# Kernel tuning notes

Measured on AMD Instinct MI355X. Metric: run time of the kernel, lower is better.

## Reference

```python
import jax, jax.numpy as jnp
import numpy as np


def setup_inputs() -> dict:
    key = jax.random.key(0)
    k1, k2, k3, k4, k5 = jax.random.split(key, 5)
    B, S, D, H, E = 4, 4096, 1024, 1024, 8  # H = per-expert hidden (fuel_dim)
    std = 0.02
    return {
        "hidden_states": jax.random.normal(k1, (B, S, D), dtype=jnp.float32),
        "gate_w": jax.random.normal(k2, (D, E), dtype=jnp.float32) * std,
        "gw": jax.random.normal(k3, (E, D, H), dtype=jnp.float32) * std,
        "pw": jax.random.normal(k4, (E, D, H), dtype=jnp.float32) * std,
        "ow": jax.random.normal(k5, (E, H, D), dtype=jnp.float32) * std,
        "top_k": 2,
    }


def reference(hidden_states, gate_w, gw, pw, ow, top_k):
    B, S, D = hidden_states.shape
    E = gate_w.shape[1]
    x = hidden_states.reshape(-1, D)  # [T, D]
    T = x.shape[0]

    # Router
    router_logits = x @ gate_w  # [T, E]
    routing_probs = jax.nn.softmax(router_logits.astype(jnp.float32), axis=-1)
    top_w, top_i = jax.lax.top_k(routing_probs, top_k)  # [T, k]
    top_w = top_w / jnp.sum(top_w, axis=-1, keepdims=True)
    top_w = top_w.astype(x.dtype)

    # Dense combine weights: zero for unselected experts -> same math as
    # the torch gather/expert/scatter loop.
    combine = jnp.zeros((T, E), dtype=x.dtype).at[
        jnp.arange(T)[:, None], top_i
    ].set(top_w)  # [T, E]

    # SwiGLU experts, batched over the expert dim.
    g = jnp.einsum('td,edh->eth', x, gw)          # [E, T, H]
    p = jnp.einsum('td,edh->eth', x, pw)          # [E, T, H]
    h = g * jax.nn.silu(p)                        # [E, T, H]
    y = jnp.einsum('eth,ehd->etd', h, ow)         # [E, T, D]
    final = jnp.einsum('etd,te->td', y, combine)  # [T, D]
    final = final.reshape(B, S, D)

    # Load-balancing loss (recomputes softmax/topk as the torch fn does)
    expert_mask = jax.nn.one_hot(top_i, E, dtype=jnp.float32)  # [T, k, E]
    tokens_per_expert = jnp.mean(expert_mask, axis=0)          # [k, E]
    router_prob_per_expert = jnp.mean(routing_probs, axis=0)   # [E]
    bl_loss = jnp.sum(tokens_per_expert * router_prob_per_expert[None, :]) * E

    return final, router_logits, bl_loss
```

## Files before the change

kernel.cpp:

```cpp
#include <hip/hip_runtime.h>
#include <hip/hip_bf16.h>
#include <cstdint>

#define T_TOK 16384
#define DDIM  1024

typedef __attribute__((ext_vector_type(8))) short bf16x8;
typedef __attribute__((ext_vector_type(4))) float f32x4;

__device__ __forceinline__ unsigned short f2bf(float f) {
  unsigned u = __builtin_bit_cast(unsigned, f);
  return (unsigned short)((u + 0x7fffu + ((u >> 16) & 1u)) >> 16);
}
__device__ __forceinline__ unsigned pk2(float a, float b) {
  return (unsigned)f2bf(a) | ((unsigned)f2bf(b) << 16);
}
__device__ __forceinline__ void gload16(const void* g, void* l) {
  typedef __attribute__((address_space(1))) const unsigned int gu32;
  typedef __attribute__((address_space(3))) unsigned int lu32;
  __builtin_amdgcn_global_load_lds((gu32*)g, (lu32*)l, 16, 0, 0);
}

#define SBAR()                        \
  __builtin_amdgcn_sched_barrier(0);  \
  __builtin_amdgcn_s_barrier();       \
  __builtin_amdgcn_sched_barrier(0)
#define WAIT_VM8()                                        \
  asm volatile("s_waitcnt vmcnt(8)" ::: "memory");        \
  __builtin_amdgcn_sched_barrier(0)
#define WAIT_VM0()                                        \
  asm volatile("s_waitcnt vmcnt(0)" ::: "memory");        \
  __builtin_amdgcn_sched_barrier(0)

__global__ __launch_bounds__(256) void convert_k(
    const float* __restrict__ gw, const float* __restrict__ pw,
    const float* __restrict__ ow, char* __restrict__ wg,
    char* __restrict__ wp, char* __restrict__ wo) {
  __shared__ float t[64][65];
  const int z = blockIdx.z;
  const int arr = z >> 3, e = z & 7;
  const float* src = (arr == 0 ? gw : arr == 1 ? pw : ow) + ((long)e << 20);
  char* dst = (arr == 0 ? wg : arr == 1 ? wp : wo) + ((long)e << 21);
  const int r0 = blockIdx.x * 64, c0 = blockIdx.y * 64;
  const int row = threadIdx.x >> 2, q = threadIdx.x & 3;
  const float4* sp = (const float4*)(src + (long)(r0 + row) * 1024 + c0 + q * 16);
  float4 v0 = sp[0], v1 = sp[1], v2 = sp[2], v3 = sp[3];
  float* tr = &t[row][q * 16];
  tr[0]=v0.x; tr[1]=v0.y; tr[2]=v0.z; tr[3]=v0.w;
  tr[4]=v1.x; tr[5]=v1.y; tr[6]=v1.z; tr[7]=v1.w;
  tr[8]=v2.x; tr[9]=v2.y; tr[10]=v2.z; tr[11]=v2.w;
  tr[12]=v3.x; tr[13]=v3.y; tr[14]=v3.z; tr[15]=v3.w;
  __syncthreads();
  const int cl = row, rq = q;
  uint4 o0, o1;
  o0.x = pk2(t[rq*16+ 0][cl], t[rq*16+ 1][cl]);
  o0.y = pk2(t[rq*16+ 2][cl], t[rq*16+ 3][cl]);
  o0.z = pk2(t[rq*16+ 4][cl], t[rq*16+ 5][cl]);
  o0.w = pk2(t[rq*16+ 6][cl], t[rq*16+ 7][cl]);
  o1.x = pk2(t[rq*16+ 8][cl], t[rq*16+ 9][cl]);
  o1.y = pk2(t[rq*16+10][cl], t[rq*16+11][cl]);
  o1.z = pk2(t[rq*16+12][cl], t[rq*16+13][cl]);
  o1.w = pk2(t[rq*16+14][cl], t[rq*16+15][cl]);
  char* dp = dst + (long)(c0 + cl) * 2048 + (long)(r0 + rq * 16) * 2;
  *(uint4*)dp = o0;
  *(uint4*)(dp + 16) = o1;
}

__global__ __launch_bounds__(256) void router_k(
    const float* __restrict__ x, const float* __restrict__ gatew,
    float* __restrict__ logitsOut, float4* __restrict__ route,
    float* __restrict__ accum, unsigned short* __restrict__ xbo) {
  __shared__ float accB[16];
  const int tid = threadIdx.x;
  if (tid < 16) accB[tid] = 0.f;
  __syncthreads();
  const int lane = tid & 63;
  const int gwave = blockIdx.x * 4 + (tid >> 6);

  for (int g = gwave; g < 4096; g += 1024) {
    const int t0 = g * 4;
    float s[4][8];
#pragma unroll
    for (int tt = 0; tt < 4; ++tt)
#pragma unroll
      for (int e = 0; e < 8; ++e) s[tt][e] = 0.f;

    for (int i = 0; i < 16; ++i) {
      int d = lane + i * 64;
      float4 w0 = *(const float4*)(gatew + d * 8);
      float4 w1 = *(const float4*)(gatew + d * 8 + 4);
#pragma unroll
      for (int tt = 0; tt < 4; ++tt) {
        float xv = x[(long)(t0 + tt) * DDIM + d];
        if (xbo) xbo[(long)(t0 + tt) * DDIM + d] = f2bf(xv);
        s[tt][0] += xv * w0.x; s[tt][1] += xv * w0.y;
        s[tt][2] += xv * w0.z; s[tt][3] += xv * w0.w;
        s[tt][4] += xv * w1.x; s[tt][5] += xv * w1.y;
        s[tt][6] += xv * w1.z; s[tt][7] += xv * w1.w;
      }
    }
#pragma unroll
    for (int m = 1; m < 64; m <<= 1)
#pragma unroll
      for (int tt = 0; tt < 4; ++tt)
#pragma unroll
        for (int e = 0; e < 8; ++e) s[tt][e] += __shfl_xor(s[tt][e], m);

    float psum[8];
#pragma unroll
    for (int e = 0; e < 8; ++e) psum[e] = 0.f;
    int i1a[4], i2a[4];
    float w1a[4], w2a[4];
#pragma unroll
    for (int tt = 0; tt < 4; ++tt) {
      float mx = s[tt][0];
#pragma unroll
      for (int e = 1; e < 8; ++e) mx = fmaxf(mx, s[tt][e]);
      float pe[8], Z = 0.f;
#pragma unroll
      for (int e = 0; e < 8; ++e) { pe[e] = __expf(s[tt][e] - mx); Z += pe[e]; }
      float inv = 1.f / Z;
#pragma unroll
      for (int e = 0; e < 8; ++e) { pe[e] *= inv; psum[e] += pe[e]; }
      int i1 = 0; float p1 = pe[0];
#pragma unroll
      for (int e = 1; e < 8; ++e) if (pe[e] > p1) { p1 = pe[e]; i1 = e; }
      int i2 = -1; float p2 = -1.f;
#pragma unroll
      for (int e = 0; e < 8; ++e)
        if (e != i1 && pe[e] > p2) { p2 = pe[e]; i2 = e; }
      float wsum = p1 + p2;
      i1a[tt] = i1; i2a[tt] = i2;
      w1a[tt] = p1 / wsum; w2a[tt] = p2 / wsum;
    }
    if (lane < 32) {
      int tt = lane >> 3, e = lane & 7;
      logitsOut[(t0 + tt) * 8 + e] = s[tt][e];
    }
    if (lane < 32 && (lane & 7) == 0) {
      int tt = lane >> 3;
      float4 rr;
      rr.x = w1a[tt]; rr.y = w2a[tt];
      rr.z = __int_as_float(i1a[tt]); rr.w = __int_as_float(i2a[tt]);
      route[t0 + tt] = rr;
    }
    if (lane < 8) {
      float c = 0.f;
#pragma unroll
      for (int tt = 0; tt < 4; ++tt)
        c += (float)(i1a[tt] == lane) + (float)(i2a[tt] == lane);
      atomicAdd(&accB[lane], psum[lane]);
      atomicAdd(&accB[8 + lane], c);
    }
  }
  __syncthreads();
  if (tid < 16) atomicAdd(&accum[tid], accB[tid]);
}

__global__ void offsets_k(const float* __restrict__ accum,
                          int* __restrict__ offs, int* __restrict__ cursor) {
  if (threadIdx.x == 0) {
    int c = 0;
#pragma unroll
    for (int e = 0; e < 8; ++e) {
      offs[e] = c; cursor[e] = c;
      c += (int)(accum[8 + e] + 0.5f);
    }
    offs[8] = c;
  }
}

__global__ __launch_bounds__(256) void scatter_k(
    const float4* __restrict__ route, int* __restrict__ cursor,
    int* __restrict__ list, float* __restrict__ wsl) {
  int t = blockIdx.x * 256 + threadIdx.x;
  float4 rr = route[t];
  int i1 = __float_as_int(rr.z), i2 = __float_as_int(rr.w);
  int s1 = atomicAdd(&cursor[i1], 1);
  list[s1] = t; wsl[s1] = rr.x;
  int s2 = atomicAdd(&cursor[i2], 1);
  list[s2] = t; wsl[s2] = rr.y;
}

template <int XB>
__global__ __launch_bounds__(512, 2) void pass1_k(
    const float* __restrict__ x, const unsigned short* __restrict__ xb,
    const char* __restrict__ wg, const char* __restrict__ wp,
    const int* __restrict__ list, const float* __restrict__ wsl,
    const int* __restrict__ offs, char* __restrict__ hw) {
  __shared__ __align__(16) char Al[2][32768];
  __shared__ __align__(16) char Bgl[2][16384];
  __shared__ __align__(16) char Bpl[2][16384];
  const int e = blockIdx.x & 7, tile = blockIdx.x >> 3;
  const int s0 = offs[e], s1 = offs[e + 1];
  const int start = s0 + tile * 256;
  if (start >= s1) return;
  const int valid = min(256, s1 - start);
  const int chunk = blockIdx.y;
  const int tid = threadIdx.x, lane = tid & 63, wid = tid >> 6;

  const int l8 = lane >> 3, seg = lane & 7;
  const unsigned inrow = ((unsigned)(seg * 16)) ^ (((unsigned)l8) << 4);

  const char* asrc[4];
  unsigned adst[4];
#pragma unroll
  for (int i = 0; i < 4; ++i) {
    int row = wid * 32 + i * 8 + l8;
    int tok = list[start + min(row, valid - 1)];
    asrc[i] = (const char*)xb + ((long)tok << 11) + inrow;
    adst[i] = (unsigned)(wid * 4096 + i * 1024);
  }
  const long wbase = ((long)e << 21) + ((long)(chunk * 128) << 11);
  const char* gsrc[2];
  const char* psrc[2];
  unsigned bdst[2];
#pragma unroll
  for (int i = 0; i < 2; ++i) {
    int h = wid * 16 + i * 8 + l8;
    gsrc[i] = wg + wbase + ((long)h << 11) + inrow;
    psrc[i] = wp + wbase + ((long)h << 11) + inrow;
    bdst[i] = (unsigned)(wid * 2048 + i * 1024);
  }

  f32x4 aG[8][2], aP[8][2];
#pragma unroll
  for (int f = 0; f < 8; ++f)
#pragma unroll
    for (int j = 0; j < 2; ++j) {
      aG[f][j] = (f32x4){0.f, 0.f, 0.f, 0.f};
      aP[f][j] = (f32x4){0.f, 0.f, 0.f, 0.f};
    }

  const int col = lane & 15, kg = lane >> 4;
  const int mb = (wid >> 2) * 128, nb = (wid & 3) * 32;

#define P1_STAGE(kb, buf)                                     \
  {                                                           \
    long ko = (long)(kb) << 7;                                \
    gload16(asrc[0] + ko, &Al[buf][adst[0]]);                 \
    gload16(asrc[1] + ko, &Al[buf][adst[1]]);                 \
    gload16(asrc[2] + ko, &Al[buf][adst[2]]);                 \
    gload16(asrc[3] + ko, &Al[buf][adst[3]]);                 \
    gload16(gsrc[0] + ko, &Bgl[buf][bdst[0]]);                \
    gload16(gsrc[1] + ko, &Bgl[buf][bdst[1]]);                \
    gload16(psrc[0] + ko, &Bpl[buf][bdst[0]]);                \
    gload16(psrc[1] + ko, &Bpl[buf][bdst[1]]);                \
  }
#define P1_COMPUTE(cur)                                                     \
  _Pragma("unroll") for (int ks = 0; ks < 2; ++ks) {                        \
    bf16x8 bg[2], bp[2];                                                    \
    _Pragma("unroll") for (int j = 0; j < 2; ++j) {                         \
      int n = nb + j * 16 + col;                                            \
      unsigned off = (unsigned)(n * 128 + ks * 64 + kg * 16) ^              \
                     (((unsigned)n & 7u) << 4);                             \
      bg[j] = *(const bf16x8*)(&Bgl[cur][0] + off);                         \
      bp[j] = *(const bf16x8*)(&Bpl[cur][0] + off);                         \
    }                                                                       \
    _Pragma("unroll") for (int f = 0; f < 8; ++f) {                         \
      int r = mb + f * 16 + col;                                            \
      bf16x8 a = *(const bf16x8*)(                                          \
          &Al[cur][0] + ((unsigned)(r * 128 + ks * 64 + kg * 16) ^          \
                         (((unsigned)r & 7u) << 4)));                       \
      _Pragma("unroll") for (int j = 0; j < 2; ++j) {                       \
        aG[f][j] = __builtin_amdgcn_mfma_f32_16x16x32_bf16(a, bg[j],        \
                                                           aG[f][j], 0, 0, 0); \
        aP[f][j] = __builtin_amdgcn_mfma_f32_16x16x32_bf16(a, bp[j],        \
                                                           aP[f][j], 0, 0, 0); \
      }                                                                     \
    }                                                                       \
  }

  if (XB) {
    P1_STAGE(0, 0);
#pragma unroll 1
    for (int kb = 0; kb < 16; ++kb) {
      const int cur = kb & 1;
      SBAR();
      if (kb < 15) {
        P1_STAGE(kb + 1, cur ^ 1);
        WAIT_VM8();
      } else {
        WAIT_VM0();
      }
      __builtin_amdgcn_s_setprio(1);
      P1_COMPUTE(cur);
      __builtin_amdgcn_s_setprio(0);
    }
  } else {
    const int sr2 = tid >> 1, q2 = tid & 1;
    const int tokS = list[start + min(sr2, valid - 1)];
    const float* axp = x + (long)tokS * DDIM + q2 * 32;
    const unsigned swzS = ((unsigned)(sr2 & 7)) << 4;
    const unsigned sbS = (unsigned)(sr2 * 128 + q2 * 64);
    for (int kb = 0; kb < 16; ++kb) {
      __syncthreads();
      {
        const float4* ap = (const float4*)(axp + kb * 64);
#pragma unroll
        for (int m = 0; m < 4; ++m) {
          float4 v0 = ap[m * 2], v1 = ap[m * 2 + 1];
          uint4 w;
          w.x = pk2(v0.x, v0.y); w.y = pk2(v0.z, v0.w);
          w.z = pk2(v1.x, v1.y); w.w = pk2(v1.z, v1.w);
          *(uint4*)(&Al[0][0] + ((sbS + m * 16) ^ swzS)) = w;
        }
        long ko = (long)kb << 7;
        gload16(gsrc[0] + ko, &Bgl[0][bdst[0]]);
        gload16(gsrc[1] + ko, &Bgl[0][bdst[1]]);
        gload16(psrc[0] + ko, &Bpl[0][bdst[0]]);
        gload16(psrc[1] + ko, &Bpl[0][bdst[1]]);
      }
      __syncthreads();
      P1_COMPUTE(0);
    }
  }

  const int rg = lane >> 4;
#pragma unroll
  for (int f = 0; f < 8; ++f) {
#pragma unroll
    for (int r = 0; r < 4; ++r) {
      int ml = mb + f * 16 + rg * 4 + r;
      if (ml < valid) {
        int slot = start + ml;
        float wv = wsl[slot];
#pragma unroll
        for (int j = 0; j < 2; ++j) {
          float g = aG[f][j][r], p = aP[f][j][r];
          float h = g * (p / (1.f + __expf(-p))) * wv;
          int hc = chunk * 128 + nb + j * 16 + col;
          *(unsigned short*)(hw + (((long)slot << 11) + (hc << 1))) = f2bf(h);
        }
      }
    }
  }
}

__global__ __launch_bounds__(512, 2) void pass2_k(
    const char* __restrict__ hw, const char* __restrict__ wo,
    const int* __restrict__ list, const int* __restrict__ offs,
    float* __restrict__ out) {
  __shared__ __align__(16) char Al[2][32768];
  __shared__ __align__(16) char Bl[2][32768];
  const int e = blockIdx.x & 7, tile = blockIdx.x >> 3;
  const int s0 = offs[e], s1 = offs[e + 1];
  const int start = s0 + tile * 256;
  if (start >= s1) return;
  const int valid = min(256, s1 - start);
  const int chunk = blockIdx.y;
  const int tid = threadIdx.x, lane = tid & 63, wid = tid >> 6;

  const int l8 = lane >> 3, seg = lane & 7;
  const unsigned inrow = ((unsigned)(seg * 16)) ^ (((unsigned)l8) << 4);

  const char* asrc[4];
  const char* bsrc[4];
  unsigned dst4[4];
#pragma unroll
  for (int i = 0; i < 4; ++i) {
    int row = wid * 32 + i * 8 + l8;
    asrc[i] = hw + ((long)(start + min(row, valid - 1)) << 11) + inrow;
    int n = wid * 32 + i * 8 + l8;
    bsrc[i] = wo + ((long)e << 21) + ((long)(chunk * 256 + n) << 11) + inrow;
    dst4[i] = (unsigned)(wid * 4096 + i * 1024);
  }

  f32x4 acc[8][4];
#pragma unroll
  for (int f = 0; f < 8; ++f)
#pragma unroll
    for (int j = 0; j < 4; ++j) acc[f][j] = (f32x4){0.f, 0.f, 0.f, 0.f};

  const int col = lane & 15, kg = lane >> 4;
  const int mb = (wid >> 2) * 128, nb = (wid & 3) * 64;

#define P2_STAGE(kb, buf)                                     \
  {                                                           \
    long ko = (long)(kb) << 7;                                \
    gload16(asrc[0] + ko, &Al[buf][dst4[0]]);                 \
    gload16(asrc[1] + ko, &Al[buf][dst4[1]]);                 \
    gload16(asrc[2] + ko, &Al[buf][dst4[2]]);                 \
    gload16(asrc[3] + ko, &Al[buf][dst4[3]]);                 \
    gload16(bsrc[0] + ko, &Bl[buf][dst4[0]]);                 \
    gload16(bsrc[1] + ko, &Bl[buf][dst4[1]]);                 \
    gload16(bsrc[2] + ko, &Bl[buf][dst4[2]]);                 \
    gload16(bsrc[3] + ko, &Bl[buf][dst4[3]]);                 \
  }

  P2_STAGE(0, 0);
#pragma unroll 1
  for (int kb = 0; kb < 16; ++kb) {
    const int cur = kb & 1;
    SBAR();
    if (kb < 15) {
      P2_STAGE(kb + 1, cur ^ 1);
      WAIT_VM8();
    } else {
      WAIT_VM0();
    }
    __builtin_amdgcn_s_setprio(1);
#pragma unroll
    for (int ks = 0; ks < 2; ++ks) {
      bf16x8 bf4[4];
#pragma unroll
      for (int j = 0; j < 4; ++j) {
        int n = nb + j * 16 + col;
        bf4[j] = *(const bf16x8*)(
            &Bl[cur][0] + ((unsigned)(n * 128 + ks * 64 + kg * 16) ^
                           (((unsigned)n & 7u) << 4)));
      }
#pragma unroll
      for (int f = 0; f < 8; ++f) {
        int r = mb + f * 16 + col;
        bf16x8 a = *(const bf16x8*)(
            &Al[cur][0] + ((unsigned)(r * 128 + ks * 64 + kg * 16) ^
                           (((unsigned)r & 7u) << 4)));
#pragma unroll
        for (int j = 0; j < 4; ++j)
          acc[f][j] = __builtin_amdgcn_mfma_f32_16x16x32_bf16(a, bf4[j],
                                                              acc[f][j], 0, 0, 0);
      }
    }
    __builtin_amdgcn_s_setprio(0);
  }

  const int rg = lane >> 4;
#pragma unroll
  for (int f = 0; f < 8; ++f) {
#pragma unroll
    for (int r = 0; r < 4; ++r) {
      int ml = mb + f * 16 + rg * 4 + r;
      if (ml < valid) {
        int token = list[start + ml];
#pragma unroll
        for (int j = 0; j < 4; ++j) {
          int c = chunk * 256 + nb + j * 16 + col;
          atomicAdd(&out[(long)token * DDIM + c], acc[f][j][r]);
        }
      }
    }
  }
}

__global__ void loss_k(const float* __restrict__ accum, float* __restrict__ out) {
  if (threadIdx.x == 0 && blockIdx.x == 0) {
    float L = 0.f;
#pragma unroll
    for (int e = 0; e < 8; ++e) L += accum[e] * accum[8 + e];
    out[0] = L * 8.f / ((float)T_TOK * (float)T_TOK);
  }
}

extern "C" void kernel_launch(void* const* d_in, const int* in_sizes, int n_in,
                              void* d_out, int out_size, void* d_ws,
                              size_t ws_size, hipStream_t stream) {
  const float* x     = (const float*)d_in[0];
  const float* gatew = (const float*)d_in[1];
  const float* gw    = (const float*)d_in[2];
  const float* pw    = (const float*)d_in[3];
  const float* ow    = (const float*)d_in[4];

  float* out       = (float*)d_out;
  float* logitsOut = out + (long)T_TOK * DDIM;
  float* lossOut   = out + (long)T_TOK * DDIM + T_TOK * 8;

  char* wsB = (char*)d_ws;
  float*  accum  = (float*)wsB;
  int*    cursor = (int*)(wsB + 64);
  int*    offs   = (int*)(wsB + 96);
  float4* route  = (float4*)(wsB + 1024);
  int*    list   = (int*)(wsB + 263168);
  float*  wsl    = (float*)(wsB + 394240);
  char*   wg     = wsB + (1l << 20);
  char*   wp     = wsB + 17825792;
  char*   wo     = wsB + 34603008;
  char*   hw     = wsB + 51380224;
  unsigned short* xb = (unsigned short*)(wsB + 118489088);
  const bool big = ws_size >= 152043520ul;

  hipMemsetAsync(d_out, 0, (size_t)out_size * 4, stream);
  hipMemsetAsync(accum, 0, 64, stream);
  convert_k<<<dim3(16, 16, 24), 256, 0, stream>>>(gw, pw, ow, wg, wp, wo);
  router_k<<<256, 256, 0, stream>>>(x, gatew, logitsOut, route, accum,
                                    big ? xb : nullptr);
  offsets_k<<<1, 64, 0, stream>>>(accum, offs, cursor);
  scatter_k<<<64, 256, 0, stream>>>(route, cursor, list, wsl);
  if (big)
    pass1_k<1><<<dim3(512, 8), 512, 0, stream>>>(x, xb, wg, wp, list, wsl,
                                                 offs, hw);
  else
    pass1_k<0><<<dim3(512, 8), 512, 0, stream>>>(x, xb, wg, wp, list, wsl,
                                                 offs, hw);
  pass2_k<<<dim3(512, 4), 512, 0, stream>>>(hw, wo, list, offs, out);
  loss_k<<<1, 64, 0, stream>>>(accum, lossOut);
}
```

Measured before the change: 694.9 us.

## Compact expert tile grid, drop double buffering, shrink pass2 tile for occupancy

Adds a cumulative per-expert tile count so the grouped GEMM grids launch only the tiles that exist (136 instead of 512 per chunk), and each block locates its expert by prefix search. Both GEMM passes drop LDS double buffering and the manual vmcnt/setprio pipelining in favour of single-buffer __syncthreads loops. Pass2's N tile is halved to 128, and launch bounds are raised to allow four blocks per CU. The aim is to raise occupancy and avoid empty blocks, at the risk of exposing global-load latency now that prefetch overlap is gone. Pass2 also does twice as many A-tile loads overall.

New measurement: 1.712 ms. 146% more time.

```diff
diff --git a/kernel.cpp b/kernel.cpp
--- a/kernel.cpp
+++ b/kernel.cpp
@@ -20,17 +20,6 @@
   typedef __attribute__((address_space(3))) unsigned int lu32;
   __builtin_amdgcn_global_load_lds((gu32*)g, (lu32*)l, 16, 0, 0);
 }
-
-#define SBAR()                        \
-  __builtin_amdgcn_sched_barrier(0);  \
-  __builtin_amdgcn_s_barrier();       \
-  __builtin_amdgcn_sched_barrier(0)
-#define WAIT_VM8()                                        \
-  asm volatile("s_waitcnt vmcnt(8)" ::: "memory");        \
-  __builtin_amdgcn_sched_barrier(0)
-#define WAIT_VM0()                                        \
-  asm volatile("s_waitcnt vmcnt(0)" ::: "memory");        \
-  __builtin_amdgcn_sched_barrier(0)
 
 __global__ __launch_bounds__(256) void convert_k(
     const float* __restrict__ gw, const float* __restrict__ pw,
@@ -158,7 +147,8 @@
 }
 
 __global__ void offsets_k(const float* __restrict__ accum,
-                          int* __restrict__ offs, int* __restrict__ cursor) {
+                          int* __restrict__ offs, int* __restrict__ cursor,
+                          int* __restrict__ cumT) {
   if (threadIdx.x == 0) {
     int c = 0;
 #pragma unroll
@@ -167,6 +157,13 @@
       c += (int)(accum[8 + e] + 0.5f);
     }
     offs[8] = c;
+    int t = 0;
+#pragma unroll
+    for (int e = 0; e < 8; ++e) {
+      cumT[e] = t;
+      t += (offs[e + 1] - offs[e] + 255) >> 8;
+    }
+    cumT[8] = t;
   }
 }
 
@@ -183,19 +180,23 @@
 }
 
 template <int XB>
-__global__ __launch_bounds__(512, 2) void pass1_k(
+__global__ __launch_bounds__(512, 4) void pass1_k(
     const float* __restrict__ x, const unsigned short* __restrict__ xb,
     const char* __restrict__ wg, const char* __restrict__ wp,
     const int* __restrict__ list, const float* __restrict__ wsl,
-    const int* __restrict__ offs, char* __restrict__ hw) {
-  __shared__ __align__(16) char Al[2][32768];
-  __shared__ __align__(16) char Bgl[2][16384];
-  __shared__ __align__(16) char Bpl[2][16384];
-  const int e = blockIdx.x & 7, tile = blockIdx.x >> 3;
-  const int s0 = offs[e], s1 = offs[e + 1];
-  const int start = s0 + tile * 256;
-  if (start >= s1) return;
-  const int valid = min(256, s1 - start);
+    const int* __restrict__ offs, const int* __restrict__ cumT,
+    char* __restrict__ hw) {
+  __shared__ __align__(16) char Al[32768];
+  __shared__ __align__(16) char Bgl[16384];
+  __shared__ __align__(16) char Bpl[16384];
+  const int b = blockIdx.x;
+  if (b >= cumT[8]) return;
+  int e = 0;
+#pragma unroll
+  for (int i = 1; i < 8; ++i) e += (b >= cumT[i]);
+  const int tile = b - cumT[e];
+  const int start = offs[e] + tile * 256;
+  const int valid = min(256, offs[e + 1] - start);
   const int chunk = blockIdx.y;
   const int tid = threadIdx.x, lane = tid & 63, wid = tid >> 6;
 
@@ -235,33 +236,33 @@
   const int col = lane & 15, kg = lane >> 4;
   const int mb = (wid >> 2) * 128, nb = (wid & 3) * 32;
 
-#define P1_STAGE(kb, buf)                                     \
+#define P1_STAGE(kb)                                          \
   {                                                           \
     long ko = (long)(kb) << 7;                                \
-    gload16(asrc[0] + ko, &Al[buf][adst[0]]);                 \
-    gload16(asrc[1] + ko, &Al[buf][adst[1]]);                 \
-    gload16(asrc[2] + ko, &Al[buf][adst[2]]);                 \
-    gload16(asrc[3] + ko, &Al[buf][adst[3]]);                 \
-    gload16(gsrc[0] + ko, &Bgl[buf][bdst[0]]);                \
-    gload16(gsrc[1] + ko, &Bgl[buf][bdst[1]]);                \
-    gload16(psrc[0] + ko, &Bpl[buf][bdst[0]]);                \
-    gload16(psrc[1] + ko, &Bpl[buf][bdst[1]]);                \
-  }
-#define P1_COMPUTE(cur)                                                     \
+    gload16(asrc[0] + ko, Al + adst[0]);                      \
+    gload16(asrc[1] + ko, Al + adst[1]);                      \
+    gload16(asrc[2] + ko, Al + adst[2]);                      \
+    gload16(asrc[3] + ko, Al + adst[3]);                      \
+    gload16(gsrc[0] + ko, Bgl + bdst[0]);                     \
+    gload16(gsrc[1] + ko, Bgl + bdst[1]);                     \
+    gload16(psrc[0] + ko, Bpl + bdst[0]);                     \
+    gload16(psrc[1] + ko, Bpl + bdst[1]);                     \
+  }
+#define P1_COMPUTE()                                                        \
   _Pragma("unroll") for (int ks = 0; ks < 2; ++ks) {                        \
     bf16x8 bg[2], bp[2];                                                    \
     _Pragma("unroll") for (int j = 0; j < 2; ++j) {                         \
       int n = nb + j * 16 + col;                                            \
       unsigned off = (unsigned)(n * 128 + ks * 64 + kg * 16) ^              \
                      (((unsigned)n & 7u) << 4);                             \
-      bg[j] = *(const bf16x8*)(&Bgl[cur][0] + off);                         \
-      bp[j] = *(const bf16x8*)(&Bpl[cur][0] + off);                         \
+      bg[j] = *(const bf16x8*)(Bgl + off);                                  \
+      bp[j] = *(const bf16x8*)(Bpl + off);                                  \
     }                                                                       \
     _Pragma("unroll") for (int f = 0; f < 8; ++f) {                         \
       int r = mb + f * 16 + col;                                            \
       bf16x8 a = *(const bf16x8*)(                                          \
-          &Al[cur][0] + ((unsigned)(r * 128 + ks * 64 + kg * 16) ^          \
-                         (((unsigned)r & 7u) << 4)));                       \
+          Al + ((unsigned)(r * 128 + ks * 64 + kg * 16) ^                   \
+                (((unsigned)r & 7u) << 4)));                                \
       _Pragma("unroll") for (int j = 0; j < 2; ++j) {                       \
         aG[f][j] = __builtin_amdgcn_mfma_f32_16x16x32_bf16(a, bg[j],        \
                                                            aG[f][j], 0, 0, 0); \
@@ -272,20 +273,12 @@
   }
 
   if (XB) {
-    P1_STAGE(0, 0);
 #pragma unroll 1
     for (int kb = 0; kb < 16; ++kb) {
-      const int cur = kb & 1;
-      SBAR();
-      if (kb < 15) {
-        P1_STAGE(kb + 1, cur ^ 1);
-        WAIT_VM8();
-      } else {
-        WAIT_VM0();
-      }
-      __builtin_amdgcn_s_setprio(1);
-      P1_COMPUTE(cur);
-      __builtin_amdgcn_s_setprio(0);
+      __syncthreads();
+      P1_STAGE(kb);
+      __syncthreads();
+      P1_COMPUTE();
     }
   } else {
     const int sr2 = tid >> 1, q2 = tid & 1;
@@ -293,6 +286,7 @@
     const float* axp = x + (long)tokS * DDIM + q2 * 32;
     const unsigned swzS = ((unsigned)(sr2 & 7)) << 4;
     const unsigned sbS = (unsigned)(sr2 * 128 + q2 * 64);
+#pragma unroll 1
     for (int kb = 0; kb < 16; ++kb) {
       __syncthreads();
       {
@@ -303,16 +297,16 @@
           uint4 w;
           w.x = pk2(v0.x, v0.y); w.y = pk2(v0.z, v0.w);
           w.z = pk2(v1.x, v1.y); w.w = pk2(v1.z, v1.w);
-          *(uint4*)(&Al[0][0] + ((sbS + m * 16) ^ swzS)) = w;
+          *(uint4*)(Al + ((sbS + m * 16) ^ swzS)) = w;
         }
         long ko = (long)kb << 7;
-        gload16(gsrc[0] + ko, &Bgl[0][bdst[0]]);
-        gload16(gsrc[1] + ko, &Bgl[0][bdst[1]]);
-        gload16(psrc[0] + ko, &Bpl[0][bdst[0]]);
-        gload16(psrc[1] + ko, &Bpl[0][bdst[1]]);
+        gload16(gsrc[0] + ko, Bgl + bdst[0]);
+        gload16(gsrc[1] + ko, Bgl + bdst[1]);
+        gload16(psrc[0] + ko, Bpl + bdst[0]);
+        gload16(psrc[1] + ko, Bpl + bdst[1]);
       }
       __syncthreads();
-      P1_COMPUTE(0);
+      P1_COMPUTE();
     }
   }
 
@@ -337,17 +331,20 @@
   }
 }
 
-__global__ __launch_bounds__(512, 2) void pass2_k(
+__global__ __launch_bounds__(512, 4) void pass2_k(
     const char* __restrict__ hw, const char* __restrict__ wo,
     const int* __restrict__ list, const int* __restrict__ offs,
-    float* __restrict__ out) {
-  __shared__ __align__(16) char Al[2][32768];
-  __shared__ __align__(16) char Bl[2][32768];
-  const int e = blockIdx.x & 7, tile = blockIdx.x >> 3;
-  const int s0 = offs[e], s1 = offs[e + 1];
-  const int start = s0 + tile * 256;
-  if (start >= s1) return;
-  const int valid = min(256, s1 - start);
+    const int* __restrict__ cumT, float* __restrict__ out) {
+  __shared__ __align__(16) char Al[32768];
+  __shared__ __align__(16) char Bl[16384];
+  const int b = blockIdx.x;
+  if (b >= cumT[8]) return;
+  int e = 0;
+#pragma unroll
+  for (int i = 1; i < 8; ++i) e += (b >= cumT[i]);
+  const int tile = b - cumT[e];
+  const int start = offs[e] + tile * 256;
+  const int valid = min(256, offs[e + 1] - start);
   const int chunk = blockIdx.y;
   const int tid = threadIdx.x, lane = tid & 63, wid = tid >> 6;
 
@@ -355,74 +352,66 @@
   const unsigned inrow = ((unsigned)(seg * 16)) ^ (((unsigned)l8) << 4);
 
   const char* asrc[4];
-  const char* bsrc[4];
-  unsigned dst4[4];
+  unsigned adst[4];
 #pragma unroll
   for (int i = 0; i < 4; ++i) {
     int row = wid * 32 + i * 8 + l8;
     asrc[i] = hw + ((long)(start + min(row, valid - 1)) << 11) + inrow;
-    int n = wid * 32 + i * 8 + l8;
-    bsrc[i] = wo + ((long)e << 21) + ((long)(chunk * 256 + n) << 11) + inrow;
-    dst4[i] = (unsigned)(wid * 4096 + i * 1024);
-  }
-
-  f32x4 acc[8][4];
+    adst[i] = (unsigned)(wid * 4096 + i * 1024);
+  }
+  const char* bsrc[2];
+  unsigned bdst[2];
+#pragma unroll
+  for (int i = 0; i < 2; ++i) {
+    int n = wid * 16 + i * 8 + l8;
+    bsrc[i] = wo + ((long)e << 21) + ((long)(chunk * 128 + n) << 11) + inrow;
+    bdst[i] = (unsigned)(wid * 2048 + i * 1024);
+  }
+
+  f32x4 acc[8][2];
 #pragma unroll
   for (int f = 0; f < 8; ++f)
 #pragma unroll
-    for (int j = 0; j < 4; ++j) acc[f][j] = (f32x4){0.f, 0.f, 0.f, 0.f};
+    for (int j = 0; j < 2; ++j) acc[f][j] = (f32x4){0.f, 0.f, 0.f, 0.f};
 
   const int col = lane & 15, kg = lane >> 4;
-  const int mb = (wid >> 2) * 128, nb = (wid & 3) * 64;
-
-#define P2_STAGE(kb, buf)                                     \
-  {                                                           \
-    long ko = (long)(kb) << 7;                                \
-    gload16(asrc[0] + ko, &Al[buf][dst4[0]]);                 \
-    gload16(asrc[1] + ko, &Al[buf][dst4[1]]);                 \
-    gload16(asrc[2] + ko, &Al[buf][dst4[2]]);                 \
-    gload16(asrc[3] + ko, &Al[buf][dst4[3]]);                 \
-    gload16(bsrc[0] + ko, &Bl[buf][dst4[0]]);                 \
-    gload16(bsrc[1] + ko, &Bl[buf][dst4[1]]);                 \
-    gload16(bsrc[2] + ko, &Bl[buf][dst4[2]]);                 \
-    gload16(bsrc[3] + ko, &Bl[buf][dst4[3]]);                 \
-  }
-
-  P2_STAGE(0, 0);
+  const int mb = (wid >> 2) * 128, nb = (wid & 3) * 32;
+
 #pragma unroll 1
   for (int kb = 0; kb < 16; ++kb) {
-    const int cur = kb & 1;
-    SBAR();
-    if (kb < 15) {
-      P2_STAGE(kb + 1, cur ^ 1);
-      WAIT_VM8();
-    } else {
-      WAIT_VM0();
-    }
-    __builtin_amdgcn_s_setprio(1);
+    __syncthreads();
+    {
+      long ko = (long)kb << 7;
+      gload16(asrc[0] + ko, Al + adst[0]);
+      gload16(asrc[1] + ko, Al + adst[1]);
+      gload16(asrc[2] + ko, Al + adst[2]);
+      gload16(asrc[3] + ko, Al + adst[3]);
+      gload16(bsrc[0] + ko, Bl + bdst[0]);
+      gload16(bsrc[1] + ko, Bl + bdst[1]);
+    }
+    __syncthreads();
 #pragma unroll
     for (int ks = 0; ks < 2; ++ks) {
-      bf16x8 bf4[4];
-#pragma unroll
-      for (int j = 0; j < 4; ++j) {
+      bf16x8 bf2[2];
+#pragma unroll
+      for (int j = 0; j < 2; ++j) {
         int n = nb + j * 16 + col;
-        bf4[j] = *(const bf16x8*)(
-            &Bl[cur][0] + ((unsigned)(n * 128 + ks * 64 + kg * 16) ^
-                           (((unsigned)n & 7u) << 4)));
+        bf2[j] = *(const bf16x8*)(
+            Bl + ((unsigned)(n * 128 + ks * 64 + kg * 16) ^
+                  (((unsigned)n & 7u) << 4)));
       }
 #pragma unroll
       for (int f = 0; f < 8; ++f) {
         int r = mb + f * 16 + col;
         bf16x8 a = *(const bf16x8*)(
-            &Al[cur][0] + ((unsigned)(r * 128 + ks * 64 + kg * 16) ^
-                           (((unsigned)r & 7u) << 4)));
-#pragma unroll
-        for (int j = 0; j < 4; ++j)
-          acc[f][j] = __builtin_amdgcn_mfma_f32_16x16x32_bf16(a, bf4[j],
+            Al + ((unsigned)(r * 128 + ks * 64 + kg * 16) ^
+                  (((unsigned)r & 7u) << 4)));
+#pragma unroll
+        for (int j = 0; j < 2; ++j)
+          acc[f][j] = __builtin_amdgcn_mfma_f32_16x16x32_bf16(a, bf2[j],
                                                               acc[f][j], 0, 0, 0);
       }
     }
-    __builtin_amdgcn_s_setprio(0);
   }
 
   const int rg = lane >> 4;
@@ -434,8 +423,8 @@
       if (ml < valid) {
         int token = list[start + ml];
 #pragma unroll
-        for (int j = 0; j < 4; ++j) {
-          int c = chunk * 256 + nb + j * 16 + col;
+        for (int j = 0; j < 2; ++j) {
+          int c = chunk * 128 + nb + j * 16 + col;
           atomicAdd(&out[(long)token * DDIM + c], acc[f][j][r]);
         }
       }
@@ -469,6 +458,7 @@
   float*  accum  = (float*)wsB;
   int*    cursor = (int*)(wsB + 64);
   int*    offs   = (int*)(wsB + 96);
+  int*    cumT   = (int*)(wsB + 160);
   float4* route  = (float4*)(wsB + 1024);
   int*    list   = (int*)(wsB + 263168);
   float*  wsl    = (float*)(wsB + 394240);
@@ -484,14 +474,14 @@
   convert_k<<<dim3(16, 16, 24), 256, 0, stream>>>(gw, pw, ow, wg, wp, wo);
   router_k<<<256, 256, 0, stream>>>(x, gatew, logitsOut, route, accum,
                                     big ? xb : nullptr);
-  offsets_k<<<1, 64, 0, stream>>>(accum, offs, cursor);
+  offsets_k<<<1, 64, 0, stream>>>(accum, offs, cursor, cumT);
   scatter_k<<<64, 256, 0, stream>>>(route, cursor, list, wsl);
   if (big)
-    pass1_k<1><<<dim3(512, 8), 512, 0, stream>>>(x, xb, wg, wp, list, wsl,
-                                                 offs, hw);
+    pass1_k<1><<<dim3(136, 8), 512, 0, stream>>>(x, xb, wg, wp, list, wsl,
+                                                 offs, cumT, hw);
   else
-    pass1_k<0><<<dim3(512, 8), 512, 0, stream>>>(x, xb, wg, wp, list, wsl,
-                                                 offs, hw);
-  pass2_k<<<dim3(512, 4), 512, 0, stream>>>(hw, wo, list, offs, out);
+    pass1_k<0><<<dim3(136, 8), 512, 0, stream>>>(x, xb, wg, wp, list, wsl,
+                                                 offs, cumT, hw);
+  pass2_k<<<dim3(136, 8), 512, 0, stream>>>(hw, wo, list, offs, cumT, out);
   loss_k<<<1, 64, 0, stream>>>(accum, lossOut);
 }
```

## Compact expert tile grid via prefix sums and split MFMA loop into barrier-synced halves

Applied to the files above, without the earlier changes.

Computes a per-expert cumulative tile count so pass1 and pass2 launch a compact grid of at most 136 tiles per chunk, instead of 512 where most blocks exit early. Each k-step's compute is now split into two halves. Each half loads A fragments into registers, waits on lgkmcnt, runs its MFMAs at raised priority, and ends at a workgroup barrier. This is meant to interleave LDS reads with MFMA across waves and cut empty-block launch overhead. The extra barriers may add sync stalls.

Measured after the change: 732.6 us. +5.4%, slower.

```diff
diff --git a/kernel.cpp b/kernel.cpp
--- a/kernel.cpp
+++ b/kernel.cpp
@@ -30,6 +30,9 @@
   __builtin_amdgcn_sched_barrier(0)
 #define WAIT_VM0()                                        \
   asm volatile("s_waitcnt vmcnt(0)" ::: "memory");        \
+  __builtin_amdgcn_sched_barrier(0)
+#define WAIT_LGKM0()                                      \
+  asm volatile("s_waitcnt lgkmcnt(0)" ::: "memory");      \
   __builtin_amdgcn_sched_barrier(0)
 
 __global__ __launch_bounds__(256) void convert_k(
@@ -158,7 +161,8 @@
 }
 
 __global__ void offsets_k(const float* __restrict__ accum,
-                          int* __restrict__ offs, int* __restrict__ cursor) {
+                          int* __restrict__ offs, int* __restrict__ cursor,
+                          int* __restrict__ cumT) {
   if (threadIdx.x == 0) {
     int c = 0;
 #pragma unroll
@@ -167,6 +171,13 @@
       c += (int)(accum[8 + e] + 0.5f);
     }
     offs[8] = c;
+    int t = 0;
+#pragma unroll
+    for (int e = 0; e < 8; ++e) {
+      cumT[e] = t;
+      t += (offs[e + 1] - offs[e] + 255) >> 8;
+    }
+    cumT[8] = t;
   }
 }
 
@@ -187,15 +198,19 @@
     const float* __restrict__ x, const unsigned short* __restrict__ xb,
     const char* __restrict__ wg, const char* __restrict__ wp,
     const int* __restrict__ list, const float* __restrict__ wsl,
-    const int* __restrict__ offs, char* __restrict__ hw) {
+    const int* __restrict__ offs, const int* __restrict__ cumT,
+    char* __restrict__ hw) {
   __shared__ __align__(16) char Al[2][32768];
   __shared__ __align__(16) char Bgl[2][16384];
   __shared__ __align__(16) char Bpl[2][16384];
-  const int e = blockIdx.x & 7, tile = blockIdx.x >> 3;
-  const int s0 = offs[e], s1 = offs[e + 1];
-  const int start = s0 + tile * 256;
-  if (start >= s1) return;
-  const int valid = min(256, s1 - start);
+  const int b = blockIdx.x;
+  if (b >= cumT[8]) return;
+  int e = 0;
+#pragma unroll
+  for (int i = 1; i < 8; ++i) e += (b >= cumT[i]);
+  const int tile = b - cumT[e];
+  const int start = offs[e] + tile * 256;
+  const int valid = min(256, offs[e + 1] - start);
   const int chunk = blockIdx.y;
   const int tid = threadIdx.x, lane = tid & 63, wid = tid >> 6;
 
@@ -247,45 +262,71 @@
     gload16(psrc[0] + ko, &Bpl[buf][bdst[0]]);                \
     gload16(psrc[1] + ko, &Bpl[buf][bdst[1]]);                \
   }
-#define P1_COMPUTE(cur)                                                     \
-  _Pragma("unroll") for (int ks = 0; ks < 2; ++ks) {                        \
-    bf16x8 bg[2], bp[2];                                                    \
-    _Pragma("unroll") for (int j = 0; j < 2; ++j) {                         \
-      int n = nb + j * 16 + col;                                            \
-      unsigned off = (unsigned)(n * 128 + ks * 64 + kg * 16) ^              \
-                     (((unsigned)n & 7u) << 4);                             \
-      bg[j] = *(const bf16x8*)(&Bgl[cur][0] + off);                         \
-      bp[j] = *(const bf16x8*)(&Bpl[cur][0] + off);                         \
-    }                                                                       \
-    _Pragma("unroll") for (int f = 0; f < 8; ++f) {                         \
-      int r = mb + f * 16 + col;                                            \
-      bf16x8 a = *(const bf16x8*)(                                          \
-          &Al[cur][0] + ((unsigned)(r * 128 + ks * 64 + kg * 16) ^          \
-                         (((unsigned)r & 7u) << 4)));                       \
-      _Pragma("unroll") for (int j = 0; j < 2; ++j) {                       \
-        aG[f][j] = __builtin_amdgcn_mfma_f32_16x16x32_bf16(a, bg[j],        \
-                                                           aG[f][j], 0, 0, 0); \
-        aP[f][j] = __builtin_amdgcn_mfma_f32_16x16x32_bf16(a, bp[j],        \
-                                                           aP[f][j], 0, 0, 0); \
-      }                                                                     \
-    }                                                                       \
-  }
 
   if (XB) {
     P1_STAGE(0, 0);
 #pragma unroll 1
     for (int kb = 0; kb < 16; ++kb) {
       const int cur = kb & 1;
-      SBAR();
       if (kb < 15) {
         P1_STAGE(kb + 1, cur ^ 1);
         WAIT_VM8();
       } else {
         WAIT_VM0();
       }
-      __builtin_amdgcn_s_setprio(1);
-      P1_COMPUTE(cur);
-      __builtin_amdgcn_s_setprio(0);
+      SBAR();
+#pragma unroll
+      for (int ks = 0; ks < 2; ++ks) {
+        bf16x8 bg[2], bp[2], af[4];
+#pragma unroll
+        for (int j = 0; j < 2; ++j) {
+          int n = nb + j * 16 + col;
+          unsigned off = (unsigned)(n * 128 + ks * 64 + kg * 16) ^
+                         (((unsigned)n & 7u) << 4);
+          bg[j] = *(const bf16x8*)(&Bgl[cur][0] + off);
+          bp[j] = *(const bf16x8*)(&Bpl[cur][0] + off);
+        }
+#pragma unroll
+        for (int f = 0; f < 4; ++f) {
+          int r = mb + f * 16 + col;
+          af[f] = *(const bf16x8*)(
+              &Al[cur][0] + ((unsigned)(r * 128 + ks * 64 + kg * 16) ^
+                             (((unsigned)r & 7u) << 4)));
+        }
+        WAIT_LGKM0();
+        __builtin_amdgcn_s_setprio(1);
+#pragma unroll
+        for (int f = 0; f < 4; ++f)
+#pragma unroll
+          for (int j = 0; j < 2; ++j) {
+            aG[f][j] = __builtin_amdgcn_mfma_f32_16x16x32_bf16(
+                af[f], bg[j], aG[f][j], 0, 0, 0);
+            aP[f][j] = __builtin_amdgcn_mfma_f32_16x16x32_bf16(
+                af[f], bp[j], aP[f][j], 0, 0, 0);
+          }
+        __builtin_amdgcn_s_setprio(0);
+        SBAR();
+#pragma unroll
+        for (int f = 0; f < 4; ++f) {
+          int r = mb + (f + 4) * 16 + col;
+          af[f] = *(const bf16x8*)(
+              &Al[cur][0] + ((unsigned)(r * 128 + ks * 64 + kg * 16) ^
+                             (((unsigned)r & 7u) << 4)));
+        }
+        WAIT_LGKM0();
+        __builtin_amdgcn_s_setprio(1);
+#pragma unroll
+        for (int f = 0; f < 4; ++f)
+#pragma unroll
+          for (int j = 0; j < 2; ++j) {
+            aG[f + 4][j] = __builtin_amdgcn_mfma_f32_16x16x32_bf16(
+                af[f], bg[j], aG[f + 4][j], 0, 0, 0);
+            aP[f + 4][j] = __builtin_amdgcn_mfma_f32_16x16x32_bf16(
+                af[f], bp[j], aP[f + 4][j], 0, 0, 0);
+          }
+        __builtin_amdgcn_s_setprio(0);
+        SBAR();
+      }
     }
   } else {
     const int sr2 = tid >> 1, q2 = tid & 1;
@@ -293,6 +334,7 @@
     const float* axp = x + (long)tokS * DDIM + q2 * 32;
     const unsigned swzS = ((unsigned)(sr2 & 7)) << 4;
     const unsigned sbS = (unsigned)(sr2 * 128 + q2 * 64);
+#pragma unroll 1
     for (int kb = 0; kb < 16; ++kb) {
       __syncthreads();
       {
@@ -312,7 +354,32 @@
         gload16(psrc[1] + ko, &Bpl[0][bdst[1]]);
       }
       __syncthreads();
-      P1_COMPUTE(0);
+#pragma unroll
+      for (int ks = 0; ks < 2; ++ks) {
+        bf16x8 bg[2], bp[2];
+#pragma unroll
+        for (int j = 0; j < 2; ++j) {
+          int n = nb + j * 16 + col;
+          unsigned off = (unsigned)(n * 128 + ks * 64 + kg * 16) ^
+                         (((unsigned)n & 7u) << 4);
+          bg[j] = *(const bf16x8*)(&Bgl[0][0] + off);
+          bp[j] = *(const bf16x8*)(&Bpl[0][0] + off);
+        }
+#pragma unroll
+        for (int f = 0; f < 8; ++f) {
+          int r = mb + f * 16 + col;
+          bf16x8 a = *(const bf16x8*)(
+              &Al[0][0] + ((unsigned)(r * 128 + ks * 64 + kg * 16) ^
+                           (((unsigned)r & 7u) << 4)));
+#pragma unroll
+          for (int j = 0; j < 2; ++j) {
+            aG[f][j] = __builtin_amdgcn_mfma_f32_16x16x32_bf16(
+                a, bg[j], aG[f][j], 0, 0, 0);
+            aP[f][j] = __builtin_amdgcn_mfma_f32_16x16x32_bf16(
+                a, bp[j], aP[f][j], 0, 0, 0);
+          }
+        }
+      }
     }
   }
 
@@ -340,14 +407,17 @@
 __global__ __launch_bounds__(512, 2) void pass2_k(
     const char* __restrict__ hw, const char* __restrict__ wo,
     const int* __restrict__ list, const int* __restrict__ offs,
-    float* __restrict__ out) {
+    const int* __restrict__ cumT, float* __restrict__ out) {
   __shared__ __align__(16) char Al[2][32768];
   __shared__ __align__(16) char Bl[2][32768];
-  const int e = blockIdx.x & 7, tile = blockIdx.x >> 3;
-  const int s0 = offs[e], s1 = offs[e + 1];
-  const int start = s0 + tile * 256;
-  if (start >= s1) return;
-  const int valid = min(256, s1 - start);
+  const int b = blockIdx.x;
+  if (b >= cumT[8]) return;
+  int e = 0;
+#pragma unroll
+  for (int i = 1; i < 8; ++i) e += (b >= cumT[i]);
+  const int tile = b - cumT[e];
+  const int start = offs[e] + tile * 256;
+  const int valid = min(256, offs[e + 1] - start);
   const int chunk = blockIdx.y;
   const int tid = threadIdx.x, lane = tid & 63, wid = tid >> 6;
 
@@ -361,8 +431,7 @@
   for (int i = 0; i < 4; ++i) {
     int row = wid * 32 + i * 8 + l8;
     asrc[i] = hw + ((long)(start + min(row, valid - 1)) << 11) + inrow;
-    int n = wid * 32 + i * 8 + l8;
-    bsrc[i] = wo + ((long)e << 21) + ((long)(chunk * 256 + n) << 11) + inrow;
+    bsrc[i] = wo + ((long)e << 21) + ((long)(chunk * 256 + row) << 11) + inrow;
     dst4[i] = (unsigned)(wid * 4096 + i * 1024);
   }
 
@@ -392,17 +461,16 @@
 #pragma unroll 1
   for (int kb = 0; kb < 16; ++kb) {
     const int cur = kb & 1;
-    SBAR();
     if (kb < 15) {
       P2_STAGE(kb + 1, cur ^ 1);
       WAIT_VM8();
     } else {
       WAIT_VM0();
     }
-    __builtin_amdgcn_s_setprio(1);
+    SBAR();
 #pragma unroll
     for (int ks = 0; ks < 2; ++ks) {
-      bf16x8 bf4[4];
+      bf16x8 bf4[4], af[4];
 #pragma unroll
       for (int j = 0; j < 4; ++j) {
         int n = nb + j * 16 + col;
@@ -411,18 +479,40 @@
                            (((unsigned)n & 7u) << 4)));
       }
 #pragma unroll
-      for (int f = 0; f < 8; ++f) {
+      for (int f = 0; f < 4; ++f) {
         int r = mb + f * 16 + col;
-        bf16x8 a = *(const bf16x8*)(
+        af[f] = *(const bf16x8*)(
             &Al[cur][0] + ((unsigned)(r * 128 + ks * 64 + kg * 16) ^
                            (((unsigned)r & 7u) << 4)));
+      }
+      WAIT_LGKM0();
+      __builtin_amdgcn_s_setprio(1);
+#pragma unroll
+      for (int f = 0; f < 4; ++f)
 #pragma unroll
         for (int j = 0; j < 4; ++j)
-          acc[f][j] = __builtin_amdgcn_mfma_f32_16x16x32_bf16(a, bf4[j],
-                                                              acc[f][j], 0, 0, 0);
-      }
-    }
-    __builtin_amdgcn_s_setprio(0);
+          acc[f][j] = __builtin_amdgcn_mfma_f32_16x16x32_bf16(
+              af[f], bf4[j], acc[f][j], 0, 0, 0);
+      __builtin_amdgcn_s_setprio(0);
+      SBAR();
+#pragma unroll
+      for (int f = 0; f < 4; ++f) {
+        int r = mb + (f + 4) * 16 + col;
+        af[f] = *(const bf16x8*)(
+            &Al[cur][0] + ((unsigned)(r * 128 + ks * 64 + kg * 16) ^
+                           (((unsigned)r & 7u) << 4)));
+      }
+      WAIT_LGKM0();
+      __builtin_amdgcn_s_setprio(1);
+#pragma unroll
+      for (int f = 0; f < 4; ++f)
+#pragma unroll
+        for (int j = 0; j < 4; ++j)
+          acc[f + 4][j] = __builtin_amdgcn_mfma_f32_16x16x32_bf16(
+              af[f], bf4[j], acc[f + 4][j], 0, 0, 0);
+      __builtin_amdgcn_s_setprio(0);
+      SBAR();
+    }
   }
 
   const int rg = lane >> 4;
@@ -469,6 +559,7 @@
   float*  accum  = (float*)wsB;
   int*    cursor = (int*)(wsB + 64);
   int*    offs   = (int*)(wsB + 96);
+  int*    cumT   = (int*)(wsB + 160);
   float4* route  = (float4*)(wsB + 1024);
   int*    list   = (int*)(wsB + 263168);
   float*  wsl    = (float*)(wsB + 394240);
@@ -484,14 +575,14 @@
   convert_k<<<dim3(16, 16, 24), 256, 0, stream>>>(gw, pw, ow, wg, wp, wo);
   router_k<<<256, 256, 0, stream>>>(x, gatew, logitsOut, route, accum,
                                     big ? xb : nullptr);
-  offsets_k<<<1, 64, 0, stream>>>(accum, offs, cursor);
+  offsets_k<<<1, 64, 0, stream>>>(accum, offs, cursor, cumT);
   scatter_k<<<64, 256, 0, stream>>>(route, cursor, list, wsl);
   if (big)
-    pass1_k<1><<<dim3(512, 8), 512, 0, stream>>>(x, xb, wg, wp, list, wsl,
-                                                 offs, hw);
+    pass1_k<1><<<dim3(136, 8), 512, 0, stream>>>(x, xb, wg, wp, list, wsl,
+                                                 offs, cumT, hw);
   else
-    pass1_k<0><<<dim3(512, 8), 512, 0, stream>>>(x, xb, wg, wp, list, wsl,
-                                                 offs, hw);
-  pass2_k<<<dim3(512, 4), 512, 0, stream>>>(hw, wo, list, offs, out);
+    pass1_k<0><<<dim3(136, 8), 512, 0, stream>>>(x, xb, wg, wp, list, wsl,
+                                                 offs, cumT, hw);
+  pass2_k<<<dim3(136, 4), 512, 0, stream>>>(hw, wo, list, offs, cumT, out);
   loss_k<<<1, 64, 0, stream>>>(accum, lossOut);
 }
```
